# Kernel tuning notes

Hardware: AMD Instinct MI355X
Metric: run time of the kernel (lower is better)

Reference implementation:

```python
import jax, jax.numpy as jnp
import numpy as np

B, H, S, D = 4, 16, 2048, 64


def setup_inputs() -> dict:
    key = jax.random.key(0)
    kq, kk, kv = jax.random.split(key, 3)
    Q = jax.random.normal(kq, (B, H, S, D), dtype=jnp.float32)
    K = jax.random.normal(kk, (B, H, S, D), dtype=jnp.float32)
    V = jax.random.normal(kv, (B, H, S, D), dtype=jnp.float32)
    # causal mask, broadcasts over (B, H); True = keep, False (==0) = mask out
    mask = jnp.tril(jnp.ones((S, S), dtype=bool))
    return {"Q": Q, "K": K, "V": V, "mask": mask}


def reference(Q, K, V, mask):
    d_k = Q.shape[-1]
    scale = 1.0 / jnp.sqrt(jnp.asarray(d_k, dtype=Q.dtype))
    # [B,H,Sq,Sk] score matrix (the module materializes this fully)
    scores = jnp.einsum('bhqd,bhkd->bhqk', Q, K) * scale
    if mask is not None:
        scores = jnp.where(mask, scores, -jnp.inf)
    attn = jax.nn.softmax(scores, axis=-1)
    return jnp.einsum('bhqk,bhkd->bhqd', attn, V)
```

## Files before the change

kernel.cpp:

```cpp
#include <hip/hip_runtime.h>
#include <math.h>

namespace {

constexpr int SEQ   = 2048;
constexpr int DH    = 64;
constexpr int KVBLK = 64;
constexpr int BH    = 64;
constexpr size_t WS_NEED = (size_t)BH * SEQ * DH * 2  * 2 ;

typedef __bf16 bf16x8 __attribute__((ext_vector_type(8)));
typedef float  f32x16 __attribute__((ext_vector_type(16)));

union FragB { bf16x8 v; unsigned u[4]; };

__device__ __forceinline__ unsigned pack2(float a, float b) {
  unsigned r;
  asm("v_cvt_pk_bf16_f32 %0, %1, %2" : "=v"(r) : "v"(a), "v"(b));
  return r;
}

__device__ __forceinline__ unsigned short bf16c(float f) {
  union { float f; unsigned u; } v; v.f = f;
  unsigned r = v.u + 0x7fffu + ((v.u >> 16) & 1u);
  return (unsigned short)(r >> 16);
}

__device__ __forceinline__ void swap32(int a, int b, int &x, int &y) {
#if __has_builtin(__builtin_amdgcn_permlane32_swap)
  auto r = __builtin_amdgcn_permlane32_swap(a, b, false, false);
  x = r[0]; y = r[1];
#else
  const bool hi = ((threadIdx.x & 63) >= 32);
  const int sa = __shfl_xor(a, 32), sb = __shfl_xor(b, 32);
  x = hi ? sb : a;
  y = hi ? b  : sa;
#endif
}

__device__ __forceinline__ float xhalf_sum(float v) {
  int x, y; swap32(__float_as_int(v), __float_as_int(v), x, y);
  return __int_as_float(x) + __int_as_float(y);
}

__device__ __forceinline__ void gload16(const void* g, void* l) {
  __builtin_amdgcn_global_load_lds(
      (const __attribute__((address_space(1))) void*)g,
      (__attribute__((address_space(3))) void*)l, 16, 0, 0);
}

__global__ __launch_bounds__(256)
void prep(const float* __restrict__ Kg, const float* __restrict__ Vg,
          unsigned short* __restrict__ wsK, unsigned short* __restrict__ wsV)
{
  const int blk = blockIdx.x;
  const int bh  = blk & 63;
  const int t   = blk >> 6;
  const int tid = threadIdx.x;

  const float* Kb = Kg + (size_t)bh * SEQ * DH;
  unsigned short* wK = wsK + (size_t)bh * SEQ * DH;
#pragma unroll
  for (int i = 0; i < 2; ++i) {
    const int kc  = tid + i * 256;
    const int row = kc >> 3, c = kc & 7;
    const int csrc = c ^ (row & 7);
    const float* s = Kb + (size_t)(t*64 + row) * DH + csrc * 8;
    float4 a = *(const float4*)s, b2 = *(const float4*)(s + 4);
    uint4 w;
    w.x = pack2(a.x, a.y);   w.y = pack2(a.z, a.w);
    w.z = pack2(b2.x, b2.y); w.w = pack2(b2.z, b2.w);
    *(uint4*)&wK[(size_t)(t*64 + row) * DH + c * 8] = w;
  }

  __shared__ unsigned short vt[64 * 64];
  const float* Vb = Vg + (size_t)bh * SEQ * DH;
  {
    const int kv = tid >> 2;
    const int d0 = (tid & 3) * 16;
    const float* s = Vb + (size_t)(t*64 + kv) * DH + d0;
#pragma unroll
    for (int e = 0; e < 16; ++e) {
      const int d = d0 + e;
      const int slot = (kv >> 3) ^ (d & 7);
      vt[d*64 + slot*8 + (kv & 7)] = bf16c(s[e]);
    }
  }
  __syncthreads();
  unsigned short* wV = wsV + (size_t)bh * SEQ * DH + (size_t)t * 4096;
#pragma unroll
  for (int i = 0; i < 2; ++i) {
    const int o = (tid + i * 256) * 8;
    *(uint4*)&wV[o] = *(const uint4*)&vt[o];
  }
}

__global__ __launch_bounds__(512, 4)
void attn_fwd(const float* __restrict__ Qg, const unsigned short* __restrict__ wsK,
              const unsigned short* __restrict__ wsV, float* __restrict__ Og)
{
  const int b   = blockIdx.x;
  const int bh  = b & 63;
  const int qi  = 15 - (b >> 6);
  const int NT  = 2 * qi + 2;

  const int tid  = threadIdx.x;
  const int wv   = tid >> 6;
  const int rw   = wv & 3;
  const int kh   = wv >> 2;
  const int lane = tid & 63;
  const int l31  = lane & 31;
  const int hi   = lane >> 5;
  const int qrel = (rw & 1) * 32 + l31;
  const int tmaxw = 2*qi + (rw >> 1);

  const float* Qp = Qg + (size_t)bh * SEQ * DH;
  const unsigned short* Kw = wsK + (size_t)bh * SEQ * DH;
  const unsigned short* Vw = wsV + (size_t)bh * SEQ * DH;
  float* Op = Og + (size_t)bh * SEQ * DH;

  __shared__ __align__(16) unsigned char smem[32768];

  const float qscale = 0.125f * 1.44269504088896f;
  FragB bq[4];
  {
    const float* src = Qp + (size_t)(qi*128 + rw*32 + l31) * DH + hi*8;
#pragma unroll
    for (int ks = 0; ks < 4; ++ks) {
      float4 f0 = *(const float4*)(src + ks*16);
      float4 f1 = *(const float4*)(src + ks*16 + 4);
      bq[ks].u[0] = pack2(f0.x*qscale, f0.y*qscale);
      bq[ks].u[1] = pack2(f0.z*qscale, f0.w*qscale);
      bq[ks].u[2] = pack2(f1.x*qscale, f1.y*qscale);
      bq[ks].u[3] = pack2(f1.z*qscale, f1.w*qscale);
    }
  }

  f32x16 oacc[2];
#pragma unroll
  for (int dt = 0; dt < 2; ++dt)
#pragma unroll
    for (int r = 0; r < 16; ++r) oacc[dt][r] = 0.f;
  float lpart = 0.f;

  auto stage = [&](int tile, int bufoff) {
    const unsigned short* gK = Kw + (size_t)tile * 4096 + wv*512 + lane*8;
    const unsigned short* gV = Vw + (size_t)tile * 4096 + wv*512 + lane*8;
    char* lb = (char*)smem + bufoff + wv*1024;
    gload16(gK, lb);
    gload16(gV, lb + 8192);
  };

  auto compute = [&](bool diag, int bufoff) {
    const unsigned short* Kl = (const unsigned short*)(smem + bufoff);
    const unsigned short* Vl = (const unsigned short*)(smem + bufoff + 8192);
    const int krow = kh*32 + l31;

    f32x16 st;
#pragma unroll
    for (int r = 0; r < 16; ++r) st[r] = 0.f;
    __builtin_amdgcn_s_setprio(1);
#pragma unroll
    for (int ks = 0; ks < 4; ++ks) {
      bf16x8 ak = *(const bf16x8*)&Kl[krow*64 + (((2*ks + hi) ^ (krow & 7)) * 8)];
      st = __builtin_amdgcn_mfma_f32_32x32x16_bf16(ak, bq[ks].v, st, 0, 0, 0);
    }
    __builtin_amdgcn_s_setprio(0);

    float p[16];
#pragma unroll
    for (int r = 0; r < 16; ++r) {
      float s = st[r];
      if (diag) {
        const int kvl = kh*32 + (r & 3) + 4*hi + 8*(r >> 2);
        if (kvl > qrel) s = -INFINITY;
      }
      const float e = exp2f(s);
      p[r] = e;
      lpart += e;
    }

    unsigned pk[8];
#pragma unroll
    for (int j2 = 0; j2 < 8; ++j2) pk[j2] = pack2(p[2*j2], p[2*j2 + 1]);

    FragB pa[2];
#pragma unroll
    for (int ks2 = 0; ks2 < 2; ++ks2) {
      const int gA = 2*ks2, gB = 2*ks2 + 1;
      int x0, y0, x1, y1;
      swap32((int)pk[2*gA],     (int)pk[2*gB],     x0, y0);
      swap32((int)pk[2*gA + 1], (int)pk[2*gB + 1], x1, y1);
      pa[ks2].u[0] = (unsigned)x0;
      pa[ks2].u[1] = (unsigned)x1;
      pa[ks2].u[2] = (unsigned)y0;
      pa[ks2].u[3] = (unsigned)y1;
    }

    __builtin_amdgcn_s_setprio(1);
#pragma unroll
    for (int dt = 0; dt < 2; ++dt) {
      const int d = dt*32 + l31;
#pragma unroll
      for (int ks2 = 0; ks2 < 2; ++ks2) {
        bf16x8 av = *(const bf16x8*)&Vl[d*64 + (((4*kh + 2*ks2 + hi) ^ (d & 7)) * 8)];
        oacc[dt] = __builtin_amdgcn_mfma_f32_32x32x16_bf16(av, pa[ks2].v, oacc[dt], 0, 0, 0);
      }
    }
    __builtin_amdgcn_s_setprio(0);
  };

  stage(0, 0);
  __syncthreads();

  for (int t = 0; t < NT; t += 2) {
    if (t + 1 < NT) stage(t + 1, 16384);
    if (t <= tmaxw) compute(t == tmaxw, 0);
    __syncthreads();
    if (t + 1 < NT) {
      if (t + 2 < NT) stage(t + 2, 0);
      if (t + 1 <= tmaxw) compute(t + 1 == tmaxw, 16384);
      __syncthreads();
    }
  }

  const int qrow = qi*128 + rw*32 + l31;
#pragma unroll
  for (int round = 0; round < 2; ++round) {
    __syncthreads();
    if ((rw >> 1) == round && kh == 1) {
      float* reg = reinterpret_cast<float*>(smem) + (rw & 1) * 4096;
      const int rb = l31 * 65;
#pragma unroll
      for (int dt = 0; dt < 2; ++dt)
#pragma unroll
        for (int g4 = 0; g4 < 4; ++g4) {
          float4 w;
          w.x = oacc[dt][4*g4 + 0]; w.y = oacc[dt][4*g4 + 1];
          w.z = oacc[dt][4*g4 + 2]; w.w = oacc[dt][4*g4 + 3];
          *(float4*)&reg[rb + dt*32 + 8*g4 + 4*hi] = w;
        }
      const float s1 = xhalf_sum(lpart);
      if (hi == 0) reg[rb + 64] = s1;
    }
    __syncthreads();
    if ((rw >> 1) == round && kh == 0) {
      const float* reg = reinterpret_cast<const float*>(smem) + (rw & 1) * 4096;
      const int rb = l31 * 65;
      const float linv = 1.0f / (xhalf_sum(lpart) + reg[rb + 64]);
      float* dst = Op + (size_t)qrow * DH;
#pragma unroll
      for (int dt = 0; dt < 2; ++dt)
#pragma unroll
        for (int g4 = 0; g4 < 4; ++g4) {
          float4 v = *(const float4*)&reg[rb + dt*32 + 8*g4 + 4*hi];
          v.x = (v.x + oacc[dt][4*g4 + 0]) * linv;
          v.y = (v.y + oacc[dt][4*g4 + 1]) * linv;
          v.z = (v.z + oacc[dt][4*g4 + 2]) * linv;
          v.w = (v.w + oacc[dt][4*g4 + 3]) * linv;
          *(float4*)&dst[dt*32 + 8*g4 + 4*hi] = v;
        }
    }
  }
}

constexpr int PADB = 72;

__global__ __launch_bounds__(256, 2)
void attn_fb(const float* __restrict__ Qg, const float* __restrict__ Kg,
             const float* __restrict__ Vg, float* __restrict__ Og)
{
  const int b   = blockIdx.x;
  const int bh  = b & 63;
  const int qi  = 31 - (b >> 6);
  const int NT  = qi + 1;
  const int tid  = threadIdx.x;
  const int wv   = tid >> 6;
  const int rw   = wv & 1;
  const int kh   = wv >> 1;
  const int lane = tid & 63;
  const int l31  = lane & 31;
  const int hi   = lane >> 5;
  const int qloc = rw * 32 + l31;

  const size_t base = (size_t)bh * SEQ * DH;
  const float* Qp = Qg + base;
  const float* Kp = Kg + base;
  const float* Vp = Vg + base;
  float*       Op = Og + base;

  __shared__ __align__(16) unsigned char smem[18432];
  auto K_lds  = reinterpret_cast<__bf16(*)[PADB]>(smem);
  auto Vt_lds = reinterpret_cast<__bf16(*)[PADB]>(smem + 9216);

  const float qscale = 0.125f * 1.44269504088896f;
  FragB bq[4];
  {
    const float* src = Qp + (size_t)(qi*64 + rw*32 + l31) * DH + hi*8;
#pragma unroll
    for (int ks = 0; ks < 4; ++ks) {
      float4 f0 = *(const float4*)(src + ks*16);
      float4 f1 = *(const float4*)(src + ks*16 + 4);
      bq[ks].u[0] = pack2(f0.x*qscale, f0.y*qscale);
      bq[ks].u[1] = pack2(f0.z*qscale, f0.w*qscale);
      bq[ks].u[2] = pack2(f1.x*qscale, f1.y*qscale);
      bq[ks].u[3] = pack2(f1.z*qscale, f1.w*qscale);
    }
  }

  float4 kr[2][2];
  float  vr[16];
  const int kc8 = tid & 7;
  const int vd  = tid & 63;
  const int vk0 = (tid >> 6) * 16;

  auto load_tile = [&](int tile) {
    const int kvb = tile * KVBLK;
#pragma unroll
    for (int p = 0; p < 2; ++p) {
      const float* s = Kp + (size_t)(kvb + 32*p + (tid >> 3)) * DH + kc8*8;
      kr[p][0] = *(const float4*)s;
      kr[p][1] = *(const float4*)(s + 4);
    }
#pragma unroll
    for (int r = 0; r < 16; ++r)
      vr[r] = Vp[(size_t)(kvb + vk0 + r) * DH + vd];
  };

  auto store_tile = [&]() {
#pragma unroll
    for (int p = 0; p < 2; ++p) {
      uint4 w;
      w.x = pack2(kr[p][0].x, kr[p][0].y); w.y = pack2(kr[p][0].z, kr[p][0].w);
      w.z = pack2(kr[p][1].x, kr[p][1].y); w.w = pack2(kr[p][1].z, kr[p][1].w);
      *reinterpret_cast<uint4*>(&K_lds[32*p + (tid >> 3)][kc8*8]) = w;
    }
    uint4 w0, w1;
    w0.x = pack2(vr[0],  vr[1]);  w0.y = pack2(vr[2],  vr[3]);
    w0.z = pack2(vr[4],  vr[5]);  w0.w = pack2(vr[6],  vr[7]);
    w1.x = pack2(vr[8],  vr[9]);  w1.y = pack2(vr[10], vr[11]);
    w1.z = pack2(vr[12], vr[13]); w1.w = pack2(vr[14], vr[15]);
    *reinterpret_cast<uint4*>(&Vt_lds[vd][vk0])     = w0;
    *reinterpret_cast<uint4*>(&Vt_lds[vd][vk0 + 8]) = w1;
  };

  f32x16 oacc[2];
#pragma unroll
  for (int dt = 0; dt < 2; ++dt)
#pragma unroll
    for (int r = 0; r < 16; ++r) oacc[dt][r] = 0.f;
  float lpart = 0.f;

  load_tile(0);
  store_tile();
  __syncthreads();

  for (int t = 0; t < NT; ++t) {
    if (t + 1 < NT) load_tile(t + 1);
    const bool diag = (t == NT - 1);

    f32x16 st;
#pragma unroll
    for (int r = 0; r < 16; ++r) st[r] = 0.f;
#pragma unroll
    for (int ks = 0; ks < 4; ++ks) {
      bf16x8 ak = *(const bf16x8*)&K_lds[kh*32 + l31][ks*16 + hi*8];
      st = __builtin_amdgcn_mfma_f32_32x32x16_bf16(ak, bq[ks].v, st, 0, 0, 0);
    }

    float p[16];
#pragma unroll
    for (int r = 0; r < 16; ++r) {
      float s = st[r];
      if (diag) {
        const int kvl = kh*32 + (r & 3) + 4*hi + 8*(r >> 2);
        if (kvl > qloc) s = -INFINITY;
      }
      const float e = exp2f(s);
      p[r] = e;
      lpart += e;
    }

    unsigned pk[8];
#pragma unroll
    for (int j2 = 0; j2 < 8; ++j2) pk[j2] = pack2(p[2*j2], p[2*j2 + 1]);

    FragB pa[2];
#pragma unroll
    for (int ks2 = 0; ks2 < 2; ++ks2) {
      const int gA = 2*ks2, gB = 2*ks2 + 1;
      int x0, y0, x1, y1;
      swap32((int)pk[2*gA],     (int)pk[2*gB],     x0, y0);
      swap32((int)pk[2*gA + 1], (int)pk[2*gB + 1], x1, y1);
      pa[ks2].u[0] = (unsigned)x0;
      pa[ks2].u[1] = (unsigned)x1;
      pa[ks2].u[2] = (unsigned)y0;
      pa[ks2].u[3] = (unsigned)y1;
    }

#pragma unroll
    for (int dt = 0; dt < 2; ++dt)
#pragma unroll
      for (int ks2 = 0; ks2 < 2; ++ks2) {
        bf16x8 av = *(const bf16x8*)&Vt_lds[dt*32 + l31][kh*32 + ks2*16 + hi*8];
        oacc[dt] = __builtin_amdgcn_mfma_f32_32x32x16_bf16(av, pa[ks2].v, oacc[dt], 0, 0, 0);
      }

    __syncthreads();
    if (t + 1 < NT) {
      store_tile();
      __syncthreads();
    }
  }

  {
    float* reg0 = reinterpret_cast<float*>(smem);
    float* reg1 = reinterpret_cast<float*>(smem + 9216);
    float* myreg = rw ? reg1 : reg0;
    const int rb = l31 * 68;

    if (kh == 1) {
#pragma unroll
      for (int dt = 0; dt < 2; ++dt)
#pragma unroll
        for (int g4 = 0; g4 < 4; ++g4) {
          float4 w;
          w.x = oacc[dt][4*g4 + 0]; w.y = oacc[dt][4*g4 + 1];
          w.z = oacc[dt][4*g4 + 2]; w.w = oacc[dt][4*g4 + 3];
          *(float4*)&myreg[rb + dt*32 + 8*g4 + 4*hi] = w;
        }
      const float s1 = xhalf_sum(lpart);
      if (hi == 0) myreg[rb + 64] = s1;
    }
    __syncthreads();
    if (kh == 0) {
      const float linv = 1.0f / (xhalf_sum(lpart) + myreg[rb + 64]);
#pragma unroll
      for (int dt = 0; dt < 2; ++dt)
#pragma unroll
        for (int g4 = 0; g4 < 4; ++g4) {
          float4 v = *(const float4*)&myreg[rb + dt*32 + 8*g4 + 4*hi];
          v.x = (v.x + oacc[dt][4*g4 + 0]) * linv;
          v.y = (v.y + oacc[dt][4*g4 + 1]) * linv;
          v.z = (v.z + oacc[dt][4*g4 + 2]) * linv;
          v.w = (v.w + oacc[dt][4*g4 + 3]) * linv;
          *(float4*)&myreg[rb + dt*32 + 8*g4 + 4*hi] = v;
        }
    }
    __syncthreads();
    {
      float* dst = Op + (size_t)(qi * 64) * DH;
#pragma unroll
      for (int i = 0; i < 4; ++i) {
        const int f   = tid + i*256;
        const int row = f >> 4;
        const int ch  = f & 15;
        const float* srcrow = (row < 32) ? (reg0 + row*68) : (reg1 + (row-32)*68);
        float4 v = *(const float4*)&srcrow[ch*4];
        *(float4*)&dst[(size_t)row*DH + ch*4] = v;
      }
    }
  }
}

}

extern "C" void kernel_launch(void* const* d_in, const int* in_sizes, int n_in,
                              void* d_out, int out_size, void* d_ws, size_t ws_size,
                              hipStream_t stream) {
  const float* Q = (const float*)d_in[0];
  const float* K = (const float*)d_in[1];
  const float* V = (const float*)d_in[2];
  float* O = (float*)d_out;
  if (ws_size >= WS_NEED) {
    unsigned short* wsK = (unsigned short*)d_ws;
    unsigned short* wsV = wsK + (size_t)BH * SEQ * DH;
    prep<<<dim3(BH * 32), dim3(256), 0, stream>>>(K, V, wsK, wsV);
    attn_fwd<<<dim3(16 * BH), dim3(512), 0, stream>>>(Q, wsK, wsV, O);
  } else {
    attn_fb<<<dim3(32 * BH), dim3(256), 0, stream>>>(Q, K, V, O);
  }
}
```

Baseline: 83.51 us.

## Drop KV-split waves: each wave processes full 64-row KV tile, halve block size

The attention kernel moves from 8 waves (4 row groups × 2 KV halves) to 4 waves. Each wave now loops over both 32-row halves of every KV tile, so the cross-wave partial-sum reduction through shared memory in the epilogue is gone. The epilogue normalizes in registers and writes through a padded LDS slab for coalesced float4 row stores. Each block now has half the waves, so it has less parallelism for latency hiding and does twice the serial MFMA/exp work per wave.

```diff
diff --git a/kernel.cpp b/kernel.cpp
--- a/kernel.cpp
+++ b/kernel.cpp
@@ -95,7 +95,7 @@
   }
 }
 
-__global__ __launch_bounds__(512, 4)
+__global__ __launch_bounds__(256, 2)
 void attn_fwd(const float* __restrict__ Qg, const unsigned short* __restrict__ wsK,
               const unsigned short* __restrict__ wsV, float* __restrict__ Og)
 {
@@ -105,13 +105,11 @@
   const int NT  = 2 * qi + 2;
 
   const int tid  = threadIdx.x;
-  const int wv   = tid >> 6;
-  const int rw   = wv & 3;
-  const int kh   = wv >> 2;
+  const int rw   = tid >> 6;
   const int lane = tid & 63;
   const int l31  = lane & 31;
   const int hi   = lane >> 5;
-  const int qrel = (rw & 1) * 32 + l31;
+  const int qloc = (rw & 1) * 32 + l31;
   const int tmaxw = 2*qi + (rw >> 1);
 
   const float* Qp = Qg + (size_t)bh * SEQ * DH;
@@ -141,73 +139,79 @@
   for (int dt = 0; dt < 2; ++dt)
 #pragma unroll
     for (int r = 0; r < 16; ++r) oacc[dt][r] = 0.f;
-  float lpart = 0.f;
+  float lp0 = 0.f, lp1 = 0.f;
 
   auto stage = [&](int tile, int bufoff) {
-    const unsigned short* gK = Kw + (size_t)tile * 4096 + wv*512 + lane*8;
-    const unsigned short* gV = Vw + (size_t)tile * 4096 + wv*512 + lane*8;
-    char* lb = (char*)smem + bufoff + wv*1024;
-    gload16(gK, lb);
-    gload16(gV, lb + 8192);
+    const unsigned short* gK = Kw + (size_t)tile * 4096 + rw*512 + lane*8;
+    const unsigned short* gV = Vw + (size_t)tile * 4096 + rw*512 + lane*8;
+    char* lb = (char*)smem + bufoff + rw*1024;
+    gload16(gK,        lb);
+    gload16(gK + 2048, lb + 4096);
+    gload16(gV,        lb + 8192);
+    gload16(gV + 2048, lb + 12288);
   };
 
   auto compute = [&](bool diag, int bufoff) {
     const unsigned short* Kl = (const unsigned short*)(smem + bufoff);
     const unsigned short* Vl = (const unsigned short*)(smem + bufoff + 8192);
-    const int krow = kh*32 + l31;
-
-    f32x16 st;
-#pragma unroll
-    for (int r = 0; r < 16; ++r) st[r] = 0.f;
-    __builtin_amdgcn_s_setprio(1);
-#pragma unroll
-    for (int ks = 0; ks < 4; ++ks) {
-      bf16x8 ak = *(const bf16x8*)&Kl[krow*64 + (((2*ks + hi) ^ (krow & 7)) * 8)];
-      st = __builtin_amdgcn_mfma_f32_32x32x16_bf16(ak, bq[ks].v, st, 0, 0, 0);
-    }
-    __builtin_amdgcn_s_setprio(0);
-
-    float p[16];
-#pragma unroll
-    for (int r = 0; r < 16; ++r) {
-      float s = st[r];
-      if (diag) {
-        const int kvl = kh*32 + (r & 3) + 4*hi + 8*(r >> 2);
-        if (kvl > qrel) s = -INFINITY;
-      }
-      const float e = exp2f(s);
-      p[r] = e;
-      lpart += e;
-    }
-
-    unsigned pk[8];
-#pragma unroll
-    for (int j2 = 0; j2 < 8; ++j2) pk[j2] = pack2(p[2*j2], p[2*j2 + 1]);
-
-    FragB pa[2];
-#pragma unroll
-    for (int ks2 = 0; ks2 < 2; ++ks2) {
-      const int gA = 2*ks2, gB = 2*ks2 + 1;
-      int x0, y0, x1, y1;
-      swap32((int)pk[2*gA],     (int)pk[2*gB],     x0, y0);
-      swap32((int)pk[2*gA + 1], (int)pk[2*gB + 1], x1, y1);
-      pa[ks2].u[0] = (unsigned)x0;
-      pa[ks2].u[1] = (unsigned)x1;
-      pa[ks2].u[2] = (unsigned)y0;
-      pa[ks2].u[3] = (unsigned)y1;
-    }
-
-    __builtin_amdgcn_s_setprio(1);
-#pragma unroll
-    for (int dt = 0; dt < 2; ++dt) {
-      const int d = dt*32 + l31;
+
+#pragma unroll
+    for (int T = 0; T < 2; ++T) {
+      const int krow = T*32 + l31;
+
+      f32x16 st;
+#pragma unroll
+      for (int r = 0; r < 16; ++r) st[r] = 0.f;
+      __builtin_amdgcn_s_setprio(1);
+#pragma unroll
+      for (int ks = 0; ks < 4; ++ks) {
+        bf16x8 ak = *(const bf16x8*)&Kl[krow*64 + (((2*ks + hi) ^ (krow & 7)) * 8)];
+        st = __builtin_amdgcn_mfma_f32_32x32x16_bf16(ak, bq[ks].v, st, 0, 0, 0);
+      }
+      __builtin_amdgcn_s_setprio(0);
+
+      float p[16];
+#pragma unroll
+      for (int r = 0; r < 16; ++r) {
+        float s = st[r];
+        if (diag) {
+          const int kvl = T*32 + (r & 3) + 4*hi + 8*(r >> 2);
+          if (kvl > qloc) s = -INFINITY;
+        }
+        const float e = exp2f(s);
+        p[r] = e;
+        if (r & 1) lp1 += e; else lp0 += e;
+      }
+
+      unsigned pk[8];
+#pragma unroll
+      for (int j2 = 0; j2 < 8; ++j2) pk[j2] = pack2(p[2*j2], p[2*j2 + 1]);
+
+      FragB pa[2];
 #pragma unroll
       for (int ks2 = 0; ks2 < 2; ++ks2) {
-        bf16x8 av = *(const bf16x8*)&Vl[d*64 + (((4*kh + 2*ks2 + hi) ^ (d & 7)) * 8)];
-        oacc[dt] = __builtin_amdgcn_mfma_f32_32x32x16_bf16(av, pa[ks2].v, oacc[dt], 0, 0, 0);
-      }
-    }
-    __builtin_amdgcn_s_setprio(0);
+        const int gA = 2*ks2, gB = 2*ks2 + 1;
+        int x0, y0, x1, y1;
+        swap32((int)pk[2*gA],     (int)pk[2*gB],     x0, y0);
+        swap32((int)pk[2*gA + 1], (int)pk[2*gB + 1], x1, y1);
+        pa[ks2].u[0] = (unsigned)x0;
+        pa[ks2].u[1] = (unsigned)x1;
+        pa[ks2].u[2] = (unsigned)y0;
+        pa[ks2].u[3] = (unsigned)y1;
+      }
+
+      __builtin_amdgcn_s_setprio(1);
+#pragma unroll
+      for (int dt = 0; dt < 2; ++dt) {
+        const int d = dt*32 + l31;
+#pragma unroll
+        for (int ks2 = 0; ks2 < 2; ++ks2) {
+          bf16x8 av = *(const bf16x8*)&Vl[d*64 + (((4*T + 2*ks2 + hi) ^ (d & 7)) * 8)];
+          oacc[dt] = __builtin_amdgcn_mfma_f32_32x32x16_bf16(av, pa[ks2].v, oacc[dt], 0, 0, 0);
+        }
+      }
+      __builtin_amdgcn_s_setprio(0);
+    }
   };
 
   stage(0, 0);
@@ -224,42 +228,36 @@
     }
   }
 
-  const int qrow = qi*128 + rw*32 + l31;
+  const float linv = 1.0f / xhalf_sum(lp0 + lp1);
+  float* smemf = reinterpret_cast<float*>(smem);
+  float* slab  = smemf + (rw & 1) * 2176;
+
 #pragma unroll
   for (int round = 0; round < 2; ++round) {
     __syncthreads();
-    if ((rw >> 1) == round && kh == 1) {
-      float* reg = reinterpret_cast<float*>(smem) + (rw & 1) * 4096;
-      const int rb = l31 * 65;
+    if ((rw >> 1) == round) {
 #pragma unroll
       for (int dt = 0; dt < 2; ++dt)
 #pragma unroll
         for (int g4 = 0; g4 < 4; ++g4) {
           float4 w;
-          w.x = oacc[dt][4*g4 + 0]; w.y = oacc[dt][4*g4 + 1];
-          w.z = oacc[dt][4*g4 + 2]; w.w = oacc[dt][4*g4 + 3];
-          *(float4*)&reg[rb + dt*32 + 8*g4 + 4*hi] = w;
+          w.x = oacc[dt][4*g4 + 0] * linv;
+          w.y = oacc[dt][4*g4 + 1] * linv;
+          w.z = oacc[dt][4*g4 + 2] * linv;
+          w.w = oacc[dt][4*g4 + 3] * linv;
+          *(float4*)&slab[l31*68 + dt*32 + 8*g4 + 4*hi] = w;
         }
-      const float s1 = xhalf_sum(lpart);
-      if (hi == 0) reg[rb + 64] = s1;
-    }
-    __syncthreads();
-    if ((rw >> 1) == round && kh == 0) {
-      const float* reg = reinterpret_cast<const float*>(smem) + (rw & 1) * 4096;
-      const int rb = l31 * 65;
-      const float linv = 1.0f / (xhalf_sum(lpart) + reg[rb + 64]);
-      float* dst = Op + (size_t)qrow * DH;
-#pragma unroll
-      for (int dt = 0; dt < 2; ++dt)
-#pragma unroll
-        for (int g4 = 0; g4 < 4; ++g4) {
-          float4 v = *(const float4*)&reg[rb + dt*32 + 8*g4 + 4*hi];
-          v.x = (v.x + oacc[dt][4*g4 + 0]) * linv;
-          v.y = (v.y + oacc[dt][4*g4 + 1]) * linv;
-          v.z = (v.z + oacc[dt][4*g4 + 2]) * linv;
-          v.w = (v.w + oacc[dt][4*g4 + 3]) * linv;
-          *(float4*)&dst[dt*32 + 8*g4 + 4*hi] = v;
-        }
+    }
+    __syncthreads();
+    if ((rw >> 1) == round) {
+      float* dst = Op + (size_t)(qi*128 + rw*32) * DH;
+#pragma unroll
+      for (int i = 0; i < 8; ++i) {
+        const int row = i*4 + (lane >> 4);
+        const int ch  = lane & 15;
+        float4 v = *(const float4*)&slab[row*68 + ch*4];
+        *(float4*)&dst[(size_t)row*DH + ch*4] = v;
+      }
     }
   }
 }
@@ -476,7 +474,7 @@
     unsigned short* wsK = (unsigned short*)d_ws;
     unsigned short* wsV = wsK + (size_t)BH * SEQ * DH;
     prep<<<dim3(BH * 32), dim3(256), 0, stream>>>(K, V, wsK, wsV);
-    attn_fwd<<<dim3(16 * BH), dim3(512), 0, stream>>>(Q, wsK, wsV, O);
+    attn_fwd<<<dim3(16 * BH), dim3(256), 0, stream>>>(Q, wsK, wsV, O);
   } else {
     attn_fb<<<dim3(32 * BH), dim3(256), 0, stream>>>(Q, K, V, O);
   }
```

Result: no change. 82.53 us (-1.2%).
